# Performance work log

Hardware: AMD Instinct MI355X
Metric: run time of the kernel (lower is better)

The kernel has to match this reference:

```python
import jax, jax.numpy as jnp
import numpy as np

LEVELS = 256

def setup_inputs() -> dict:
    key = jax.random.key(0)
    # pixel values in [0, 256), already uint8-range ints (original casts to uint8)
    x = jax.random.randint(key, (64, 786432), 0, LEVELS, dtype=jnp.int32)
    return {"x": x}

def reference(x):
    # Per-sample 256-bin histogram over all pixels (cv2.calcHist equivalent),
    # implemented as an atomic-add scatter per row via vmap.
    B = x.shape[0]

    def hist_one(row):  # row: [N] int32 in [0, LEVELS)
        return jnp.zeros((LEVELS,), dtype=jnp.float32).at[row].add(1.0)

    hist = jax.vmap(hist_one)(x)  # [B, LEVELS]
    # cv2.calcHist returns shape (LEVELS, 1); assignment into a (LEVELS, LEVELS)
    # slot broadcasts the histogram column across all 256 columns.
    out = jnp.broadcast_to(hist[:, :, None], (B, LEVELS, LEVELS))
    # original returns a list containing this single stacked tensor
    return out
```

## Files before the change

kernel.cpp:

```cpp
#include <hip/hip_runtime.h>

#define LEVELS 256
#define NROWS 64
#define ROWLEN 786432
#define CHUNKS 32
#define CHUNK_ELEMS (ROWLEN / CHUNKS)
#define BLOCK 256
#define WAVES (BLOCK / 64)

__global__ __launch_bounds__(256) void hist_partial_kernel(const int* __restrict__ x,
                                                           unsigned int* __restrict__ ws) {
    __shared__ unsigned int lhist[WAVES][LEVELS];

    const int row   = blockIdx.y;
    const int chunk = blockIdx.x;
    const int tid   = threadIdx.x;
    const int wave  = tid >> 6;

    unsigned int* flat = &lhist[0][0];
    for (int i = tid; i < WAVES * LEVELS; i += BLOCK) flat[i] = 0u;
    __syncthreads();

    const int4* xr = (const int4*)(x + (long)row * ROWLEN + (long)chunk * CHUNK_ELEMS);
    const int n4 = CHUNK_ELEMS / 4;
    unsigned int* h = lhist[wave];
    for (int i = tid; i < n4; i += 2 * BLOCK) {
        int4 a = xr[i];
        int4 b = xr[i + BLOCK];
        atomicAdd(&h[a.x & 255], 1u);
        atomicAdd(&h[a.y & 255], 1u);
        atomicAdd(&h[a.z & 255], 1u);
        atomicAdd(&h[a.w & 255], 1u);
        atomicAdd(&h[b.x & 255], 1u);
        atomicAdd(&h[b.y & 255], 1u);
        atomicAdd(&h[b.z & 255], 1u);
        atomicAdd(&h[b.w & 255], 1u);
    }
    __syncthreads();

    unsigned int* dst = ws + ((long)(row * CHUNKS + chunk)) * LEVELS;
    for (int bin = tid; bin < LEVELS; bin += BLOCK) {
        unsigned int s = 0u;
        #pragma unroll
        for (int w = 0; w < WAVES; ++w) s += lhist[w][bin];
        dst[bin] = s;
    }
}

__global__ __launch_bounds__(256) void reduce_broadcast_kernel(const unsigned int* __restrict__ ws,
                                                               float* __restrict__ out) {
    const int b    = blockIdx.x >> 6;
    const int vg   = blockIdx.x & 63;
    const int wave = threadIdx.x >> 6;
    const int lane = threadIdx.x & 63;
    const int bin  = vg * 4 + wave;

    unsigned int v = ws[((long)(b * CHUNKS) + (lane & 31)) * LEVELS + bin];
    #pragma unroll
    for (int m = 1; m <= 16; m <<= 1) v += (unsigned int)__shfl_xor((int)v, m);
    float val = (float)v;

    float4* dst = (float4*)(out + ((long)b * LEVELS + bin) * LEVELS);
    dst[lane] = make_float4(val, val, val, val);
}

extern "C" void kernel_launch(void* const* d_in, const int* in_sizes, int n_in,
                              void* d_out, int out_size, void* d_ws, size_t ws_size,
                              hipStream_t stream) {
    const int* x = (const int*)d_in[0];
    float* out = (float*)d_out;
    unsigned int* ws = (unsigned int*)d_ws;

    dim3 grid(CHUNKS, NROWS);
    hist_partial_kernel<<<grid, BLOCK, 0, stream>>>(x, ws);

    reduce_broadcast_kernel<<<NROWS * 64, BLOCK, 0, stream>>>(ws, out);
}
```

Baseline: 277.1 us.

## Deepen histogram load unroll and restructure reduce-broadcast with nontemporal stores

The histogram kernel now issues four 16-byte loads per thread per iteration instead of two, putting more memory requests in flight before the LDS atomics. The reduce-broadcast kernel is reorganised so each block handles 32 bins of one row. It sums chunk partials across 8 groups through shared memory, then writes the 32x256 broadcast tile with nontemporal vector stores, using fewer and larger blocks. This aims to cut redundant partial reads and cache pollution from the large output write, at the cost of extra syncs and fewer blocks in the second kernel.

```diff
diff --git a/kernel.cpp b/kernel.cpp
--- a/kernel.cpp
+++ b/kernel.cpp
@@ -7,6 +7,9 @@
 #define CHUNK_ELEMS (ROWLEN / CHUNKS)
 #define BLOCK 256
 #define WAVES (BLOCK / 64)
+
+typedef int   v4i __attribute__((ext_vector_type(4)));
+typedef float v4f __attribute__((ext_vector_type(4)));
 
 __global__ __launch_bounds__(256) void hist_partial_kernel(const int* __restrict__ x,
                                                            unsigned int* __restrict__ ws) {
@@ -21,12 +24,14 @@
     for (int i = tid; i < WAVES * LEVELS; i += BLOCK) flat[i] = 0u;
     __syncthreads();
 
-    const int4* xr = (const int4*)(x + (long)row * ROWLEN + (long)chunk * CHUNK_ELEMS);
+    const v4i* xr = (const v4i*)(x + (long)row * ROWLEN + (long)chunk * CHUNK_ELEMS);
     const int n4 = CHUNK_ELEMS / 4;
     unsigned int* h = lhist[wave];
-    for (int i = tid; i < n4; i += 2 * BLOCK) {
-        int4 a = xr[i];
-        int4 b = xr[i + BLOCK];
+    for (int i = tid; i < n4; i += 4 * BLOCK) {
+        v4i a = xr[i];
+        v4i b = xr[i + BLOCK];
+        v4i c = xr[i + 2 * BLOCK];
+        v4i d = xr[i + 3 * BLOCK];
         atomicAdd(&h[a.x & 255], 1u);
         atomicAdd(&h[a.y & 255], 1u);
         atomicAdd(&h[a.z & 255], 1u);
@@ -35,6 +40,14 @@
         atomicAdd(&h[b.y & 255], 1u);
         atomicAdd(&h[b.z & 255], 1u);
         atomicAdd(&h[b.w & 255], 1u);
+        atomicAdd(&h[c.x & 255], 1u);
+        atomicAdd(&h[c.y & 255], 1u);
+        atomicAdd(&h[c.z & 255], 1u);
+        atomicAdd(&h[c.w & 255], 1u);
+        atomicAdd(&h[d.x & 255], 1u);
+        atomicAdd(&h[d.y & 255], 1u);
+        atomicAdd(&h[d.z & 255], 1u);
+        atomicAdd(&h[d.w & 255], 1u);
     }
     __syncthreads();
 
@@ -49,19 +62,41 @@
 
 __global__ __launch_bounds__(256) void reduce_broadcast_kernel(const unsigned int* __restrict__ ws,
                                                                float* __restrict__ out) {
-    const int b    = blockIdx.x >> 6;
-    const int vg   = blockIdx.x & 63;
-    const int wave = threadIdx.x >> 6;
-    const int lane = threadIdx.x & 63;
-    const int bin  = vg * 4 + wave;
+    __shared__ unsigned int red[8][32];
+    __shared__ float vals[32];
 
-    unsigned int v = ws[((long)(b * CHUNKS) + (lane & 31)) * LEVELS + bin];
+    const int row  = blockIdx.x >> 3;
+    const int bq   = blockIdx.x & 7;
+    const int tid  = threadIdx.x;
+    const int wave = tid >> 6;
+    const int lane = tid & 63;
+    const int g    = wave * 2 + (lane >> 5);
+    const int binl = lane & 31;
+    const int bin  = bq * 32 + binl;
+
+    const unsigned int* base = ws + (long)row * CHUNKS * LEVELS + bin;
+    unsigned int s = 0u;
     #pragma unroll
-    for (int m = 1; m <= 16; m <<= 1) v += (unsigned int)__shfl_xor((int)v, m);
-    float val = (float)v;
+    for (int c = g; c < CHUNKS; c += 8) s += base[(long)c * LEVELS];
 
-    float4* dst = (float4*)(out + ((long)b * LEVELS + bin) * LEVELS);
-    dst[lane] = make_float4(val, val, val, val);
+    red[g][binl] = s;
+    __syncthreads();
+
+    if (tid < 32) {
+        unsigned int t = 0u;
+        #pragma unroll
+        for (int gg = 0; gg < 8; ++gg) t += red[gg][tid];
+        vals[tid] = (float)t;
+    }
+    __syncthreads();
+
+    v4f* dst = (v4f*)(out + ((long)row * LEVELS + bq * 32) * LEVELS);
+    #pragma unroll
+    for (int i = tid; i < 32 * (LEVELS / 4); i += BLOCK) {
+        float v = vals[i >> 6];
+        v4f f = {v, v, v, v};
+        __builtin_nontemporal_store(f, &dst[i]);
+    }
 }
 
 extern "C" void kernel_launch(void* const* d_in, const int* in_sizes, int n_in,
@@ -74,5 +109,5 @@
     dim3 grid(CHUNKS, NROWS);
     hist_partial_kernel<<<grid, BLOCK, 0, stream>>>(x, ws);
 
-    reduce_broadcast_kernel<<<NROWS * 64, BLOCK, 0, stream>>>(ws, out);
+    reduce_broadcast_kernel<<<NROWS * 8, BLOCK, 0, stream>>>(ws, out);
 }
```

Measured after the change: 276.7 us. No clear change (-0.1%).
